# Performance work log

Measured on AMD Instinct MI355X. Metric: run time of the kernel, lower is better.

Reference implementation:

```python
import jax, jax.numpy as jnp
import numpy as np
import math

N, E, D, H, C, G = 100000, 1600000, 256, 256, 4, 512
LN_EPS = 1e-5


def _pe(n, d):
    # sinusoidal positional encoding, rows = node index
    pos = jnp.arange(n, dtype=jnp.float32)[:, None]                      # [n,1]
    div = jnp.exp(jnp.arange(0, d, 2, dtype=jnp.float32) * (-math.log(10000.0) / d))  # [d/2]
    ang = pos * div                                                      # [n,d/2]
    return jnp.stack([jnp.sin(ang), jnp.cos(ang)], axis=-1).reshape(n, d)


def setup_inputs() -> dict:
    key = jax.random.key(0)
    ks = jax.random.split(key, 24)
    w = lambda k, shp: (jax.random.normal(k, shp, jnp.float32) * 0.05)
    inp = {
        "x": jax.random.normal(ks[0], (N, D), jnp.float32),
        "W_ft": w(ks[1], (D, H)), "b_ft": jnp.zeros((H,), jnp.float32),
        "ln_g": jnp.ones((H,), jnp.float32), "ln_b": jnp.zeros((H,), jnp.float32),
        "W_g0": w(ks[2], (H, H)), "b_g0": jnp.zeros((H,), jnp.float32),
        "W_g1": w(ks[3], (H, H)), "b_g1": jnp.zeros((H,), jnp.float32),
        "W_g2": w(ks[4], (H, H)), "b_g2": jnp.zeros((H,), jnp.float32),
        "W_c0": w(ks[5], (H, H)), "b_c0": jnp.zeros((H,), jnp.float32),
        "W_c1": w(ks[6], (H, H // 2)), "b_c1": jnp.zeros((H // 2,), jnp.float32),
        "W_c2": w(ks[7], (H // 2, C)), "b_c2": jnp.zeros((C,), jnp.float32),
        "edge_index": jax.random.randint(ks[8], (2, E), 0, N, dtype=jnp.int32),
        "batch": jnp.sort(jax.random.randint(ks[9], (N,), 0, G, dtype=jnp.int32)),
    }
    return inp


def reference(x, W_ft, b_ft, ln_g, ln_b, W_g0, b_g0, W_g1, b_g1, W_g2, b_g2,
              W_c0, b_c0, W_c1, b_c1, W_c2, b_c2, edge_index, batch):
    # feature transform: Linear + ReLU + Dropout(eval) + LayerNorm
    h = jax.nn.relu(x @ W_ft + b_ft)
    mu = jnp.mean(h, axis=-1, keepdims=True)
    var = jnp.mean(jnp.square(h - mu), axis=-1, keepdims=True)
    h = (h - mu) * jax.lax.rsqrt(var + LN_EPS) * ln_g + ln_b
    # temporal positional encoding (intended per-node add)
    h = h + _pe(N, H)
    # GCN layers (PyG GCNConv: self-loops + symmetric degree norm + scatter-add)
    loops = jnp.arange(N, dtype=edge_index.dtype)
    src = jnp.concatenate([edge_index[0], loops])
    dst = jnp.concatenate([edge_index[1], loops])
    deg = jax.ops.segment_sum(jnp.ones_like(dst, dtype=h.dtype), dst, num_segments=N)
    dinv = jnp.where(deg > 0, jax.lax.rsqrt(jnp.maximum(deg, 1.0)), 0.0)
    norm = (dinv[src] * dinv[dst])[:, None]                              # [E+N,1]
    for W, b in ((W_g0, b_g0), (W_g1, b_g1), (W_g2, b_g2)):
        m = (h @ W)[src] * norm                                          # gather + scale
        h = jax.nn.relu(jax.ops.segment_sum(m, dst, num_segments=N) + b)
    # global mean pool per graph
    sums = jax.ops.segment_sum(h, batch, num_segments=G)
    cnts = jax.ops.segment_sum(jnp.ones((N,), h.dtype), batch, num_segments=G)
    pooled = sums / jnp.maximum(cnts, 1.0)[:, None]                      # [G,H]
    # classifier MLP
    z = jax.nn.relu(pooled @ W_c0 + b_c0)
    z = jax.nn.relu(z @ W_c1 + b_c1)
    return z @ W_c2 + b_c2                                               # [G,C]
```

## Files before the change

kernel.cpp:

```cpp
#include <hip/hip_runtime.h>
#include <math.h>


typedef __attribute__((ext_vector_type(8))) _Float16 half8;
typedef __attribute__((ext_vector_type(4))) float floatx4;
typedef __attribute__((ext_vector_type(8))) unsigned short us8;

union HU { _Float16 h; unsigned short u; };

static __device__ __forceinline__ unsigned short f2h(float f) {
    HU x; x.h = (_Float16)f; return x.u;
}
static __device__ __forceinline__ float h2f(unsigned short s) {
    HU x; x.u = s; return (float)x.h;
}

static __device__ __forceinline__ void gl_lds16(const void* g, void* l) {
    __builtin_amdgcn_global_load_lds(
        (const __attribute__((address_space(1))) unsigned int*)(g),
        (__attribute__((address_space(3))) unsigned int*)(l), 16, 0, 0);
}

__global__ void tg_splitB(const float* __restrict__ W0, const float* __restrict__ W1,
                          const float* __restrict__ W2, const float* __restrict__ W3,
                          unsigned short* __restrict__ B0, unsigned short* __restrict__ B1,
                          unsigned short* __restrict__ B2, unsigned short* __restrict__ B3)
{
    const float* Ws[4] = {W0, W1, W2, W3};
    unsigned short* Bs[4] = {B0, B1, B2, B3};
    const float* W = Ws[blockIdx.z];
    unsigned short* Bt = Bs[blockIdx.z];

    __shared__ float T[64][68];
    const int tk = blockIdx.x * 64, tn = blockIdx.y * 64;
    const int t = threadIdx.x;
#pragma unroll
    for (int j = 0; j < 4; ++j) {
        const int idx = t + 256 * j;
        const int k = idx >> 4, c4 = (idx & 15) * 4;
        const float4 v = *(const float4*)&W[(size_t)(tk + k) * 256 + tn + c4];
        T[k][c4] = v.x; T[k][c4 + 1] = v.y; T[k][c4 + 2] = v.z; T[k][c4 + 3] = v.w;
    }
    __syncthreads();
#pragma unroll
    for (int j = 0; j < 4; ++j) {
        const int idx = t + 256 * j;
        const int n = idx >> 4, q = (idx & 15) * 4;
        unsigned short hh[4], ll[4];
#pragma unroll
        for (int i = 0; i < 4; ++i) {
            const float f = T[q + i][n];
            hh[i] = f2h(f);
            ll[i] = f2h(f - h2f(hh[i]));
        }
        uint2 hp, lp;
        hp.x = (unsigned)hh[0] | ((unsigned)hh[1] << 16);
        hp.y = (unsigned)hh[2] | ((unsigned)hh[3] << 16);
        lp.x = (unsigned)ll[0] | ((unsigned)ll[1] << 16);
        lp.y = (unsigned)ll[2] | ((unsigned)ll[3] << 16);
        unsigned short* row = Bt + (size_t)(tn + n) * 512;
        *(uint2*)&row[tk + q]       = hp;
        *(uint2*)&row[256 + tk + q] = lp;
    }
}

__global__ __launch_bounds__(256, 2)
void tg_ft_ln(const float* __restrict__ x, const unsigned short* __restrict__ Bt,
              const float* __restrict__ bias, const float* __restrict__ lng,
              const float* __restrict__ lnb, unsigned short* __restrict__ hh, int N)
{
    __shared__ unsigned short sAh[128 * 64];
    __shared__ unsigned short sAl[128 * 64];
    __shared__ unsigned short sB[256 * 64];
    __shared__ float sStats[128][2][2];

    const int t = threadIdx.x;
    const int w = t >> 6, lane = t & 63;
    const int quad = lane >> 4, l16 = lane & 15;
    const int wr = w >> 1, wc = w & 1;
    const int row0 = blockIdx.x * 128;

    floatx4 acc[4][8];
#pragma unroll
    for (int i = 0; i < 4; ++i)
#pragma unroll
        for (int j = 0; j < 8; ++j) acc[i][j] = (floatx4){0.f, 0.f, 0.f, 0.f};

    const int arow = t >> 1;
    const int ahalf = t & 1;
    const int srow = lane >> 3;
    const int kgx  = (lane & 7) ^ srow;
    const int rsw  = l16 & 7;

    for (int k4 = 0; k4 < 4; ++k4) {
        const int ka = k4 * 64;
        if (k4) __syncthreads();
        {
            const int grow = row0 + arow;
            const bool ok = grow < N;
            const float* xp = x + (size_t)grow * 256 + ka + ahalf * 32;
#pragma unroll
            for (int j = 0; j < 4; ++j) {
                const int kg = ahalf * 4 + j;
                float4 v0 = {0.f, 0.f, 0.f, 0.f}, v1 = {0.f, 0.f, 0.f, 0.f};
                if (ok) {
                    v0 = *(const float4*)(xp + j * 8);
                    v1 = *(const float4*)(xp + j * 8 + 4);
                }
                const float f[8] = {v0.x, v0.y, v0.z, v0.w, v1.x, v1.y, v1.z, v1.w};
                us8 hi, lo;
#pragma unroll
                for (int i = 0; i < 8; ++i) {
                    hi[i] = f2h(f[i]);
                    lo[i] = f2h(f[i] - h2f(hi[i]));
                }
                const int ad = arow * 64 + ((kg ^ (arow & 7)) << 3);
                *(us8*)&sAh[ad] = hi;
                *(us8*)&sAl[ad] = lo;
            }
        }
#pragma unroll
        for (int i = 0; i < 8; ++i) {
            const int rr = w * 64 + i * 8;
            gl_lds16(Bt + (size_t)(rr + srow) * 512 + ka + kgx * 8, &sB[rr * 64]);
        }
        __syncthreads();
#pragma unroll
        for (int ks = 0; ks < 2; ++ks) {
            const int kq = ks * 4 + quad;
            half8 afh[4], afl[4];
#pragma unroll
            for (int rt = 0; rt < 4; ++rt) {
                const int r = wr * 64 + rt * 16 + l16;
                const int off = r * 64 + ((kq ^ rsw) << 3);
                afh[rt] = *(const half8*)&sAh[off];
                afl[rt] = *(const half8*)&sAl[off];
            }
#pragma unroll
            for (int cb = 0; cb < 2; ++cb) {
                half8 bfr[4];
#pragma unroll
                for (int c4 = 0; c4 < 4; ++c4) {
                    const int n = wc * 128 + (cb * 4 + c4) * 16 + l16;
                    bfr[c4] = *(const half8*)&sB[n * 64 + ((kq ^ rsw) << 3)];
                }
#pragma unroll
                for (int c4 = 0; c4 < 4; ++c4)
#pragma unroll
                    for (int rt = 0; rt < 4; ++rt) {
                        acc[rt][cb * 4 + c4] = __builtin_amdgcn_mfma_f32_16x16x32_f16(
                            afh[rt], bfr[c4], acc[rt][cb * 4 + c4], 0, 0, 0);
                        acc[rt][cb * 4 + c4] = __builtin_amdgcn_mfma_f32_16x16x32_f16(
                            afl[rt], bfr[c4], acc[rt][cb * 4 + c4], 0, 0, 0);
                    }
            }
        }
        __syncthreads();
#pragma unroll
        for (int i = 0; i < 8; ++i) {
            const int rr = w * 64 + i * 8;
            gl_lds16(Bt + (size_t)(rr + srow) * 512 + 256 + ka + kgx * 8, &sB[rr * 64]);
        }
        __syncthreads();
#pragma unroll
        for (int ks = 0; ks < 2; ++ks) {
            const int kq = ks * 4 + quad;
            half8 afh[4];
#pragma unroll
            for (int rt = 0; rt < 4; ++rt) {
                const int r = wr * 64 + rt * 16 + l16;
                afh[rt] = *(const half8*)&sAh[r * 64 + ((kq ^ rsw) << 3)];
            }
#pragma unroll
            for (int cb = 0; cb < 2; ++cb) {
                half8 bfr[4];
#pragma unroll
                for (int c4 = 0; c4 < 4; ++c4) {
                    const int n = wc * 128 + (cb * 4 + c4) * 16 + l16;
                    bfr[c4] = *(const half8*)&sB[n * 64 + ((kq ^ rsw) << 3)];
                }
#pragma unroll
                for (int c4 = 0; c4 < 4; ++c4)
#pragma unroll
                    for (int rt = 0; rt < 4; ++rt)
                        acc[rt][cb * 4 + c4] = __builtin_amdgcn_mfma_f32_16x16x32_f16(
                            afh[rt], bfr[c4], acc[rt][cb * 4 + c4], 0, 0, 0);
            }
        }
    }

    float bs[8];
#pragma unroll
    for (int ct = 0; ct < 8; ++ct) bs[ct] = bias[wc * 128 + ct * 16 + l16];
#pragma unroll
    for (int rt = 0; rt < 4; ++rt) {
#pragma unroll
        for (int i = 0; i < 4; ++i) {
            float s = 0.f, q = 0.f;
#pragma unroll
            for (int ct = 0; ct < 8; ++ct) {
                const float v = fmaxf(acc[rt][ct][i] + bs[ct], 0.f);
                s += v; q += v * v;
            }
#pragma unroll
            for (int m = 1; m < 16; m <<= 1) {
                s += __shfl_xor(s, m, 64);
                q += __shfl_xor(q, m, 64);
            }
            if (l16 == 0) {
                const int rl = wr * 64 + rt * 16 + quad * 4 + i;
                sStats[rl][wc][0] = s;
                sStats[rl][wc][1] = q;
            }
        }
    }
    __syncthreads();

    float* sC = (float*)sB;
    const float bias_c = bias[t];
    const float g_c = lng[t];
    const float b_c = lnb[t];
    const float cexp = -0.035977892078031970f;
    const float dv_c = expf((float)(t & ~1) * cexp);
    const float phase = (t & 1) ? 1.5707963267948966f : 0.f;

#pragma unroll
    for (int rt = 0; rt < 4; ++rt) {
#pragma unroll
        for (int i = 0; i < 4; ++i) {
            const int srl = wr * 16 + quad * 4 + i;
#pragma unroll
            for (int ct = 0; ct < 8; ++ct)
                sC[srl * 256 + wc * 128 + ct * 16 + l16] = acc[rt][ct][i];
        }
        __syncthreads();
        for (int q = 0; q < 32; ++q) {
            const int rl = (q >> 4) * 64 + rt * 16 + (q & 15);
            const int gr = row0 + rl;
            if (gr < N) {
                const float sum = sStats[rl][0][0] + sStats[rl][1][0];
                const float sq  = sStats[rl][0][1] + sStats[rl][1][1];
                const float mu  = sum * (1.f / 256.f);
                const float var = sq * (1.f / 256.f) - mu * mu;
                const float rstd = 1.f / sqrtf(var + 1e-5f);
                const float v = fmaxf(sC[q * 256 + t] + bias_c, 0.f);
                const float nrm = (v - mu) * rstd * g_c + b_c;
                const float pe = sinf((float)gr * dv_c + phase);
                hh[(size_t)gr * 256 + t] = f2h(nrm + pe);
            }
        }
        __syncthreads();
    }
}

__global__ __launch_bounds__(256, 3)
void tg_gemm(const unsigned short* __restrict__ Ph,
             const unsigned short* __restrict__ Bt,
             const float* __restrict__ rowscale,
             unsigned short* __restrict__ out)
{
    __shared__ unsigned short sA[128 * 64], sB[128 * 64];

    const int t = threadIdx.x;
    const int w = t >> 6, lane = t & 63;
    const int quad = lane >> 4, l16 = lane & 15;
    const int wr = w >> 1, wc = w & 1;

    const int nwg = gridDim.x;
    const int swq = nwg >> 3, swr = nwg & 7;
    const int xcd = blockIdx.x & 7, oidx = blockIdx.x >> 3;
    const int lg = (xcd < swr ? xcd * (swq + 1)
                              : swr * (swq + 1) + (xcd - swr) * swq) + oidx;
    const int row0 = (lg >> 1) * 128;
    const int col0 = (lg & 1) * 128;

    floatx4 acc[4][4];
#pragma unroll
    for (int i = 0; i < 4; ++i)
#pragma unroll
        for (int j = 0; j < 4; ++j) acc[i][j] = (floatx4){0.f, 0.f, 0.f, 0.f};

    const int srow = lane >> 3;
    const int kgx  = (lane & 7) ^ srow;
    const int rsw  = l16 & 7;

    for (int c = 0; c < 8; ++c) {
        const int ka = (c >> 1) << 6;
        const int kb = ((c & 1) << 8) + ka;
        const bool stA = !(c & 1);
        if (c) __syncthreads();
#pragma unroll
        for (int i = 0; i < 4; ++i) {
            const int rr = w * 32 + i * 8;
            if (stA)
                gl_lds16(Ph + (size_t)(row0 + rr + srow) * 256 + ka + kgx * 8, &sA[rr * 64]);
            gl_lds16(Bt + (size_t)(col0 + rr + srow) * 512 + kb + kgx * 8, &sB[rr * 64]);
        }
        __syncthreads();
#pragma unroll
        for (int ks = 0; ks < 2; ++ks) {
            const int kq = ks * 4 + quad;
            half8 af[4], bfr[4];
#pragma unroll
            for (int rt = 0; rt < 4; ++rt) {
                const int r = wr * 64 + rt * 16 + l16;
                af[rt] = *(const half8*)&sA[r * 64 + ((kq ^ rsw) << 3)];
            }
#pragma unroll
            for (int ct = 0; ct < 4; ++ct) {
                const int n = wc * 64 + ct * 16 + l16;
                bfr[ct] = *(const half8*)&sB[n * 64 + ((kq ^ rsw) << 3)];
            }
#pragma unroll
            for (int ct = 0; ct < 4; ++ct)
#pragma unroll
                for (int rt = 0; rt < 4; ++rt)
                    acc[rt][ct] = __builtin_amdgcn_mfma_f32_16x16x32_f16(
                        af[rt], bfr[ct], acc[rt][ct], 0, 0, 0);
        }
    }

#pragma unroll
    for (int rt = 0; rt < 4; ++rt) {
#pragma unroll
        for (int i = 0; i < 4; ++i) {
            const int gr = row0 + wr * 64 + rt * 16 + quad * 4 + i;
            const float s = rowscale[gr];
#pragma unroll
            for (int ct = 0; ct < 4; ++ct) {
                const int gc = col0 + wc * 64 + ct * 16 + l16;
                out[(size_t)gr * 256 + gc] = f2h(acc[rt][ct][i] * s);
            }
        }
    }
}

__global__ void tg_count(const int* __restrict__ dst, int* __restrict__ deg,
                         int* __restrict__ perm, int E)
{
    const int e = blockIdx.x * blockDim.x + threadIdx.x;
    if (e < E) perm[e] = atomicAdd(&deg[dst[e]], 1);
}

__global__ void tg_dinv(const int* __restrict__ deg, float* __restrict__ dinv, int N)
{
    const int i = blockIdx.x * blockDim.x + threadIdx.x;
    if (i < N) dinv[i] = 1.f / sqrtf((float)(deg[i] + 1));
}

__global__ void tg_scan1(const int* __restrict__ cnt, int* __restrict__ out,
                         int* __restrict__ sums, int N)
{
    __shared__ int tmp[1024];
    const int t = threadIdx.x;
    const int gid = blockIdx.x * 1024 + t;
    const int v = (gid < N) ? cnt[gid] : 0;
    tmp[t] = v;
    __syncthreads();
    for (int o = 1; o < 1024; o <<= 1) {
        const int add = (t >= o) ? tmp[t - o] : 0;
        __syncthreads();
        tmp[t] += add;
        __syncthreads();
    }
    if (gid < N) out[gid] = tmp[t] - v;
    if (t == 1023) sums[blockIdx.x] = tmp[t];
}

__global__ void tg_scan2(int* __restrict__ sums, int nb)
{
    __shared__ int tmp[1024];
    const int t = threadIdx.x;
    const int v = (t < nb) ? sums[t] : 0;
    tmp[t] = v;
    __syncthreads();
    for (int o = 1; o < 1024; o <<= 1) {
        const int add = (t >= o) ? tmp[t - o] : 0;
        __syncthreads();
        tmp[t] += add;
        __syncthreads();
    }
    if (t < nb) sums[t] = tmp[t] - v;
}

__global__ void tg_scan3(int* __restrict__ rowptr, const int* __restrict__ offs,
                         int N, int E)
{
    const int gid = blockIdx.x * 1024 + threadIdx.x;
    if (gid < N) rowptr[gid] += offs[gid >> 10];
    else if (gid == N) rowptr[N] = E;
}

__global__ void tg_fill(const int* __restrict__ src, const int* __restrict__ dst,
                        const int* __restrict__ rowptr, const int* __restrict__ perm,
                        int* __restrict__ col, int E)
{
    const int e = blockIdx.x * blockDim.x + threadIdx.x;
    if (e >= E) return;
    col[rowptr[dst[e]] + perm[e]] = src[e];
}

__global__ void tg_aggregate_h(const unsigned short* __restrict__ hwpb,
                               const int* __restrict__ rowptr, const int* __restrict__ col,
                               const float* __restrict__ dinv, const float* __restrict__ bias,
                               unsigned short* __restrict__ hh, int N)
{
    const int gt = blockIdx.x * blockDim.x + threadIdx.x;
    const int row = gt >> 5;
    if (row >= N) return;
    const int hl = gt & 31;
    const int c = hl * 8;

    const unsigned short* base = hwpb + c;
    const int beg = rowptr[row], end = rowptr[row + 1];

    const us8 sv = *(const us8*)(base + (size_t)row * 256);
    float a[8];
#pragma unroll
    for (int j = 0; j < 8; ++j) a[j] = h2f(sv[j]);

    int p = beg;
    int rem = end - beg;
    int c0[8];
    if (rem >= 8) {
#pragma unroll
        for (int u = 0; u < 8; ++u) c0[u] = col[p + u];
    }
    while (rem >= 8) {
        int c1[8];
        const bool more = rem >= 16;
        if (more) {
#pragma unroll
            for (int u = 0; u < 8; ++u) c1[u] = col[p + 8 + u];
        }
        us8 v[8];
#pragma unroll
        for (int u = 0; u < 8; ++u)
            v[u] = *(const us8*)(base + (size_t)c0[u] * 256);
#pragma unroll
        for (int u = 0; u < 8; ++u)
#pragma unroll
            for (int j = 0; j < 8; ++j) a[j] += h2f(v[u][j]);
        if (more) {
#pragma unroll
            for (int u = 0; u < 8; ++u) c0[u] = c1[u];
        }
        p += 8; rem -= 8;
    }
    if (rem > 0) {
        const int last = end - 1;
        int ci[8];
#pragma unroll
        for (int u = 0; u < 8; ++u) {
            const int pp = (p + u < last) ? p + u : last;
            ci[u] = col[pp];
        }
        us8 v[8];
#pragma unroll
        for (int u = 0; u < 8; ++u)
            v[u] = *(const us8*)(base + (size_t)(u < rem ? ci[u] : row) * 256);
#pragma unroll
        for (int u = 0; u < 8; ++u) {
            if (u < rem) {
#pragma unroll
                for (int j = 0; j < 8; ++j) a[j] += h2f(v[u][j]);
            }
        }
    }

    const float di = dinv[row];
    const float4 b0 = *(const float4*)&bias[c];
    const float4 b1 = *(const float4*)&bias[c + 4];
    us8 o;
    o[0] = f2h(fmaxf(di * a[0] + b0.x, 0.f));
    o[1] = f2h(fmaxf(di * a[1] + b0.y, 0.f));
    o[2] = f2h(fmaxf(di * a[2] + b0.z, 0.f));
    o[3] = f2h(fmaxf(di * a[3] + b0.w, 0.f));
    o[4] = f2h(fmaxf(di * a[4] + b1.x, 0.f));
    o[5] = f2h(fmaxf(di * a[5] + b1.y, 0.f));
    o[6] = f2h(fmaxf(di * a[6] + b1.z, 0.f));
    o[7] = f2h(fmaxf(di * a[7] + b1.w, 0.f));
    *(us8*)&hh[(size_t)row * 256 + c] = o;
}

__global__ void tg_ranges(const int* __restrict__ batch, int* __restrict__ starts,
                          int N, int G)
{
    const int g = blockIdx.x * blockDim.x + threadIdx.x;
    if (g > G) return;
    int lo = 0, hi = N;
    while (lo < hi) {
        const int mid = (lo + hi) >> 1;
        if (batch[mid] < g) lo = mid + 1; else hi = mid;
    }
    starts[g] = lo;
}

__global__ void tg_pool(const unsigned short* __restrict__ hh,
                        const int* __restrict__ starts, float* __restrict__ pooled, int G)
{
    __shared__ float sh[4][64][4];
    const int g = blockIdx.x;
    const int t = threadIdx.x;
    const int wv = t >> 6, lane = t & 63;
    const int c = lane * 4;
    const int beg = starts[g], end = starts[g + 1];
    float s0 = 0.f, s1 = 0.f, s2 = 0.f, s3 = 0.f;
    for (int r = beg + wv; r < end; r += 4) {
        const ushort4 vh = *(const ushort4*)&hh[(size_t)r * 256 + c];
        s0 += h2f(vh.x); s1 += h2f(vh.y); s2 += h2f(vh.z); s3 += h2f(vh.w);
    }
    sh[wv][lane][0] = s0; sh[wv][lane][1] = s1;
    sh[wv][lane][2] = s2; sh[wv][lane][3] = s3;
    __syncthreads();
    if (t < 64) {
        const float inv = 1.f / fmaxf((float)(end - beg), 1.f);
        float4 o;
        o.x = (sh[0][t][0] + sh[1][t][0] + sh[2][t][0] + sh[3][t][0]) * inv;
        o.y = (sh[0][t][1] + sh[1][t][1] + sh[2][t][1] + sh[3][t][1]) * inv;
        o.z = (sh[0][t][2] + sh[1][t][2] + sh[2][t][2] + sh[3][t][2]) * inv;
        o.w = (sh[0][t][3] + sh[1][t][3] + sh[2][t][3] + sh[3][t][3]) * inv;
        *(float4*)&pooled[(size_t)g * 256 + t * 4] = o;
    }
}

__global__ void tg_mlp(const float* __restrict__ A, const float* __restrict__ B,
                       const float* __restrict__ bias, float* __restrict__ Cout,
                       int M, int K, int Nc, int do_relu)
{
    const int idx = blockIdx.x * blockDim.x + threadIdx.x;
    if (idx >= M * Nc) return;
    const int m = idx / Nc;
    const int n = idx - m * Nc;
    float acc = 0.f;
    for (int k = 0; k < K; ++k) acc += A[(size_t)m * K + k] * B[(size_t)k * Nc + n];
    acc += bias[n];
    Cout[idx] = do_relu ? fmaxf(acc, 0.f) : acc;
}

extern "C" void kernel_launch(void* const* d_in, const int* in_sizes, int n_in,
                              void* d_out, int out_size, void* d_ws, size_t ws_size,
                              hipStream_t stream)
{
    const float* x    = (const float*)d_in[0];
    const float* W_ft = (const float*)d_in[1];
    const float* b_ft = (const float*)d_in[2];
    const float* ln_g = (const float*)d_in[3];
    const float* ln_b = (const float*)d_in[4];
    const float* W_g[3] = {(const float*)d_in[5], (const float*)d_in[7], (const float*)d_in[9]};
    const float* b_g[3] = {(const float*)d_in[6], (const float*)d_in[8], (const float*)d_in[10]};
    const float* W_c0 = (const float*)d_in[11];
    const float* b_c0 = (const float*)d_in[12];
    const float* W_c1 = (const float*)d_in[13];
    const float* b_c1 = (const float*)d_in[14];
    const float* W_c2 = (const float*)d_in[15];
    const float* b_c2 = (const float*)d_in[16];
    const int*   edge  = (const int*)d_in[17];
    const int*   batch = (const int*)d_in[18];

    const int N    = in_sizes[18];
    const int E    = in_sizes[17] / 2;
    const int Mpad = (N + 127) & ~127;
    const int H2   = in_sizes[14];
    const int Cc   = in_sizes[15] / H2;
    const int G    = out_size / Cc;

    const int* srcI = edge;
    const int* dstI = edge + E;

    size_t off = 0;
    auto alloc = [&](size_t bytes) {
        char* p = (char*)d_ws + off;
        off = (off + bytes + 255) & ~(size_t)255;
        return p;
    };
    unsigned short* hh   = (unsigned short*)alloc((size_t)Mpad * 256 * 2);
    unsigned short* hwpb = (unsigned short*)alloc((size_t)Mpad * 256 * 2);
    float* dinv   = (float*)alloc((size_t)Mpad * 4);
    int*   deg    = (int*)alloc((size_t)Mpad * 4);
    int*   rowptr = (int*)alloc((size_t)(N + 1) * 4);
    int*   perm   = (int*)alloc((size_t)E * 4);
    int*   col    = (int*)alloc((size_t)E * 4);
    int*   bsums  = (int*)alloc(1024 * 4);
    int*   starts = (int*)alloc((size_t)(G + 1) * 4);
    float* pooled = (float*)alloc((size_t)G * 256 * 4);
    float* z0     = (float*)alloc((size_t)G * 256 * 4);
    float* z1     = (float*)alloc((size_t)G * H2 * 4);
    unsigned short* Bt[4];
    for (int i = 0; i < 4; ++i)
        Bt[i] = (unsigned short*)alloc((size_t)256 * 512 * 2);
    (void)ws_size; (void)n_in;

    hipMemsetAsync(deg, 0, (size_t)Mpad * 4, stream);
    hipMemsetAsync(hh + (size_t)N * 256, 0, (size_t)(Mpad - N) * 256 * 2, stream);

    tg_splitB<<<dim3(4, 4, 4), dim3(256), 0, stream>>>(
        W_ft, W_g[0], W_g[1], W_g[2], Bt[0], Bt[1], Bt[2], Bt[3]);

    tg_ft_ln<<<dim3(Mpad / 128), dim3(256), 0, stream>>>(
        x, Bt[0], b_ft, ln_g, ln_b, hh, N);

    tg_count<<<dim3((E + 255) / 256), dim3(256), 0, stream>>>(dstI, deg, perm, E);
    tg_dinv<<<dim3((Mpad + 255) / 256), dim3(256), 0, stream>>>(deg, dinv, Mpad);
    const int NB = (N + 1023) / 1024;
    tg_scan1<<<dim3(NB), dim3(1024), 0, stream>>>(deg, rowptr, bsums, N);
    tg_scan2<<<dim3(1), dim3(1024), 0, stream>>>(bsums, NB);
    tg_scan3<<<dim3((N + 1024) / 1024), dim3(1024), 0, stream>>>(rowptr, bsums, N, E);
    tg_fill<<<dim3((E + 255) / 256), dim3(256), 0, stream>>>(srcI, dstI, rowptr, perm, col, E);

    const int nbx = (Mpad / 128) * 2;
    for (int l = 0; l < 3; ++l) {
        tg_gemm<<<dim3(nbx), dim3(256), 0, stream>>>(hh, Bt[l + 1], dinv, hwpb);
        tg_aggregate_h<<<dim3((N + 7) / 8), dim3(256), 0, stream>>>(hwpb, rowptr, col, dinv,
                                                                    b_g[l], hh, N);
    }

    tg_ranges<<<dim3((G + 256) / 256), dim3(256), 0, stream>>>(batch, starts, N, G);
    tg_pool<<<dim3(G), dim3(256), 0, stream>>>(hh, starts, pooled, G);

    tg_mlp<<<dim3((G * 256 + 255) / 256), dim3(256), 0, stream>>>(pooled, W_c0, b_c0, z0, G, 256, 256, 1);
    tg_mlp<<<dim3((G * H2 + 255) / 256), dim3(256), 0, stream>>>(z0, W_c1, b_c1, z1, G, 256, H2, 1);
    tg_mlp<<<dim3((G * Cc + 255) / 256), dim3(256), 0, stream>>>(z1, W_c2, b_c2, (float*)d_out, G, H2, Cc, 0);
}
```

Baseline: 1.091 ms.

## Fuse LayerNorm epilogue in registers with fast trig and earlier B prefetch

Measured after the change: 1.061 ms. 1.03x faster.

```diff
diff --git a/kernel.cpp b/kernel.cpp
--- a/kernel.cpp
+++ b/kernel.cpp
@@ -19,6 +19,16 @@
     __builtin_amdgcn_global_load_lds(
         (const __attribute__((address_space(1))) unsigned int*)(g),
         (__attribute__((address_space(3))) unsigned int*)(l), 16, 0, 0);
+}
+
+static __device__ __forceinline__ float cw_trig(float ang, bool is_cos) {
+    const float i2pi = 0.15915494309189535f;
+    const float k = rintf(ang * i2pi);
+    float r = fmaf(k, -6.28125f, ang);
+    r = fmaf(k, -1.9352436065673828e-3f, r);
+    r = fmaf(k, -6.3573019e-8f, r);
+    const float rv = r * i2pi;
+    return is_cos ? __builtin_amdgcn_cosf(rv) : __builtin_amdgcn_sinf(rv);
 }
 
 __global__ void tg_splitB(const float* __restrict__ W0, const float* __restrict__ W1,
@@ -73,6 +83,7 @@
     __shared__ unsigned short sAl[128 * 64];
     __shared__ unsigned short sB[256 * 64];
     __shared__ float sStats[128][2][2];
+    __shared__ float sDiv[128];
 
     const int t = threadIdx.x;
     const int w = t >> 6, lane = t & 63;
@@ -80,6 +91,8 @@
     const int wr = w >> 1, wc = w & 1;
     const int row0 = blockIdx.x * 128;
 
+    if (t < 128) sDiv[t] = expf((float)(2 * t) * -0.035977892078031970f);
+
     floatx4 acc[4][8];
 #pragma unroll
     for (int i = 0; i < 4; ++i)
@@ -95,6 +108,11 @@
     for (int k4 = 0; k4 < 4; ++k4) {
         const int ka = k4 * 64;
         if (k4) __syncthreads();
+#pragma unroll
+        for (int i = 0; i < 8; ++i) {
+            const int rr = w * 64 + i * 8;
+            gl_lds16(Bt + (size_t)(rr + srow) * 512 + ka + kgx * 8, &sB[rr * 64]);
+        }
         {
             const int grow = row0 + arow;
             const bool ok = grow < N;
@@ -119,11 +137,6 @@
                 *(us8*)&sAl[ad] = lo;
             }
         }
-#pragma unroll
-        for (int i = 0; i < 8; ++i) {
-            const int rr = w * 64 + i * 8;
-            gl_lds16(Bt + (size_t)(rr + srow) * 512 + ka + kgx * 8, &sB[rr * 64]);
-        }
         __syncthreads();
 #pragma unroll
         for (int ks = 0; ks < 2; ++ks) {
@@ -189,9 +202,14 @@
         }
     }
 
-    float bs[8];
-#pragma unroll
-    for (int ct = 0; ct < 8; ++ct) bs[ct] = bias[wc * 128 + ct * 16 + l16];
+    float bs[8], gs[8], bv[8], dv[8];
+#pragma unroll
+    for (int ct = 0; ct < 8; ++ct) {
+        const int gc = wc * 128 + ct * 16 + l16;
+        bs[ct] = bias[gc]; gs[ct] = lng[gc]; bv[ct] = lnb[gc];
+        dv[ct] = sDiv[gc >> 1];
+    }
+
 #pragma unroll
     for (int rt = 0; rt < 4; ++rt) {
 #pragma unroll
@@ -216,40 +234,29 @@
     }
     __syncthreads();
 
-    float* sC = (float*)sB;
-    const float bias_c = bias[t];
-    const float g_c = lng[t];
-    const float b_c = lnb[t];
-    const float cexp = -0.035977892078031970f;
-    const float dv_c = expf((float)(t & ~1) * cexp);
-    const float phase = (t & 1) ? 1.5707963267948966f : 0.f;
-
+    const bool is_cos = (l16 & 1);
 #pragma unroll
     for (int rt = 0; rt < 4; ++rt) {
 #pragma unroll
         for (int i = 0; i < 4; ++i) {
-            const int srl = wr * 16 + quad * 4 + i;
-#pragma unroll
-            for (int ct = 0; ct < 8; ++ct)
-                sC[srl * 256 + wc * 128 + ct * 16 + l16] = acc[rt][ct][i];
-        }
-        __syncthreads();
-        for (int q = 0; q < 32; ++q) {
-            const int rl = (q >> 4) * 64 + rt * 16 + (q & 15);
+            const int rl = wr * 64 + rt * 16 + quad * 4 + i;
             const int gr = row0 + rl;
-            if (gr < N) {
-                const float sum = sStats[rl][0][0] + sStats[rl][1][0];
-                const float sq  = sStats[rl][0][1] + sStats[rl][1][1];
-                const float mu  = sum * (1.f / 256.f);
-                const float var = sq * (1.f / 256.f) - mu * mu;
-                const float rstd = 1.f / sqrtf(var + 1e-5f);
-                const float v = fmaxf(sC[q * 256 + t] + bias_c, 0.f);
-                const float nrm = (v - mu) * rstd * g_c + b_c;
-                const float pe = sinf((float)gr * dv_c + phase);
-                hh[(size_t)gr * 256 + t] = f2h(nrm + pe);
-            }
-        }
-        __syncthreads();
+            if (gr >= N) continue;
+            const float sum = sStats[rl][0][0] + sStats[rl][1][0];
+            const float sq  = sStats[rl][0][1] + sStats[rl][1][1];
+            const float mu  = sum * (1.f / 256.f);
+            const float var = sq * (1.f / 256.f) - mu * mu;
+            const float rstd = 1.f / sqrtf(var + 1e-5f);
+            const float rf = (float)gr;
+            unsigned short* orow = hh + (size_t)gr * 256 + wc * 128 + l16;
+#pragma unroll
+            for (int ct = 0; ct < 8; ++ct) {
+                const float v = fmaxf(acc[rt][ct][i] + bs[ct], 0.f);
+                const float nrm = (v - mu) * rstd * gs[ct] + bv[ct];
+                const float pe = cw_trig(rf * dv[ct], is_cos);
+                orow[ct * 16] = f2h(nrm + pe);
+            }
+        }
     }
 }
 
```
